# Optimization experiments

Hardware: AMD Instinct MI355X
Metric: run time of the kernel (lower is better)

Reference implementation:

```python
import jax, jax.numpy as jnp
import numpy as np

N, C, E, K = 50000, 128, 640000, 40  # nodes, feat dim, edges, classes
EPS = 1e-5


def setup_inputs() -> dict:
    key = jax.random.key(0)
    ks = jax.random.split(key, 8)
    s = 1.0 / np.sqrt(C)
    return {
        "x": jax.random.normal(ks[0], (N, C), jnp.float32),
        "edge_index": jax.random.randint(ks[1], (2, E), 0, N, dtype=jnp.int32),
        "W_conv": jax.random.normal(ks[2], (C, C), jnp.float32) * s,
        "b_conv": jnp.zeros((C,), jnp.float32),
        "gamma": jnp.ones((C,), jnp.float32),
        "beta": jnp.zeros((C,), jnp.float32),
        "W_fc": jax.random.normal(ks[3], (C, K), jnp.float32) * s,
        "b_fc": jnp.zeros((K,), jnp.float32),
    }


def reference(x, edge_index, W_conv, b_conv, gamma, beta, W_fc, b_fc):
    n = x.shape[0]
    loops = jnp.arange(n, dtype=edge_index.dtype)
    src = jnp.concatenate([edge_index[0], loops])  # add self-loops (PyG default)
    dst = jnp.concatenate([edge_index[1], loops])
    # symmetric normalization: deg^{-1/2}[src] * deg^{-1/2}[dst]
    deg = jax.ops.segment_sum(jnp.ones_like(dst, jnp.float32), dst, num_segments=n)
    dinv = jax.lax.rsqrt(jnp.maximum(deg, 1.0))  # deg >= 1 with self-loops
    norm = dinv[src] * dinv[dst]  # [E+N]
    h = x @ W_conv  # [N, C] transform before propagate (GCNConv)
    agg = jax.ops.segment_sum(h[src] * norm[:, None], dst, num_segments=n) + b_conv
    a = jax.nn.relu(agg) * x  # dropout = identity (eval mode); elementwise mul with residual
    mu = jnp.mean(a, axis=-1, keepdims=True)
    var = jnp.mean((a - mu) ** 2, axis=-1, keepdims=True)
    ln = (a - mu) * jax.lax.rsqrt(var + EPS) * gamma + beta
    return (ln + x) @ W_fc + b_fc
```

## Files before the change

### kernel.cpp

```cpp
#include <hip/hip_runtime.h>

#define C_DIM 128
#define EPS 1e-5f
#define DEG_CAP 64
#define NSCAT 625

typedef __attribute__((ext_vector_type(8))) short short8;
typedef __attribute__((ext_vector_type(4))) float f32x4;

__device__ __forceinline__ unsigned bf16rn(float f) {
    unsigned u = __float_as_uint(f);
    return (u + 0x7fffu + ((u >> 16) & 1u)) >> 16;
}
__device__ __forceinline__ unsigned pack_bf16(float lo, float hi) {
    return bf16rn(lo) | (bf16rn(hi) << 16);
}
__device__ __forceinline__ float blo(unsigned u) { return __uint_as_float(u << 16); }
__device__ __forceinline__ float bhi(unsigned u) { return __uint_as_float(u & 0xffff0000u); }

__global__ __launch_bounds__(256, 4) void fat(const float* __restrict__ x,
                                              const float* __restrict__ W,
                                              unsigned* __restrict__ hb,
                                              const float* __restrict__ Wfc,
                                              unsigned short* __restrict__ WT,
                                              const int* __restrict__ esrc,
                                              const int* __restrict__ edst,
                                              int* __restrict__ cnt,
                                              int* __restrict__ bsrc,
                                              int n, int e, int g1) {
    __shared__ float xT[32][133];
    __shared__ float ws[32][133];
    int b = blockIdx.x;
    int t = threadIdx.x;

    if (b < NSCAT) {
        const int S = NSCAT * 256;
        int i0 = b * 256 + t;
        int i1 = i0 + S, i2 = i1 + S, i3 = i2 + S;
        int d0 = edst[i0], d1 = edst[i1], d2 = edst[i2], d3 = edst[i3];
        int s0 = esrc[i0], s1 = esrc[i1], s2 = esrc[i2], s3 = esrc[i3];
        int p0 = atomicAdd(&cnt[d0], 1);
        int p1 = atomicAdd(&cnt[d1], 1);
        int p2 = atomicAdd(&cnt[d2], 1);
        int p3 = atomicAdd(&cnt[d3], 1);
        if (p0 < DEG_CAP) __builtin_nontemporal_store(s0, &bsrc[(long)d0 * DEG_CAP + p0]);
        if (p1 < DEG_CAP) __builtin_nontemporal_store(s1, &bsrc[(long)d1 * DEG_CAP + p1]);
        if (p2 < DEG_CAP) __builtin_nontemporal_store(s2, &bsrc[(long)d2 * DEG_CAP + p2]);
        if (p3 < DEG_CAP) __builtin_nontemporal_store(s3, &bsrc[(long)d3 * DEG_CAP + p3]);
    } else if (b < NSCAT + g1) {
        int r0 = (b - NSCAT) * 128;
        int w = t >> 6, lane = t & 63;
        int wr = (w >> 1) * 64, wc = (w & 1) * 64;
        int lr = (lane >> 3) * 8, lc = (lane & 7) * 8;
        float acc[8][8] = {};
        for (int kc = 0; kc < 128; kc += 32) {
            __syncthreads();
#pragma unroll
            for (int i = 0; i < 4; i++) {
                int idx = t + i * 256;
                int r = idx >> 3;
                int k4 = (idx & 7) << 2;
                float4 v = make_float4(0.f, 0.f, 0.f, 0.f);
                if (r0 + r < n) v = *(const float4*)&x[(long)(r0 + r) * C_DIM + kc + k4];
                xT[k4 + 0][r] = v.x; xT[k4 + 1][r] = v.y; xT[k4 + 2][r] = v.z; xT[k4 + 3][r] = v.w;
            }
#pragma unroll
            for (int i = 0; i < 4; i++) {
                int idx = t + i * 256;
                int k = idx >> 5;
                int c4 = (idx & 31) << 2;
                *(float4*)&ws[k][c4] = *(const float4*)&W[(long)(kc + k) * C_DIM + c4];
            }
            __syncthreads();
#pragma unroll 4
            for (int k = 0; k < 32; k++) {
                float a[8], bb[8];
                *(float4*)&a[0] = *(float4*)&xT[k][wr + lr];
                *(float4*)&a[4] = *(float4*)&xT[k][wr + lr + 4];
                *(float4*)&bb[0] = *(float4*)&ws[k][wc + lc];
                *(float4*)&bb[4] = *(float4*)&ws[k][wc + lc + 4];
#pragma unroll
                for (int i = 0; i < 8; i++)
#pragma unroll
                    for (int j = 0; j < 8; j++)
                        acc[i][j] += a[i] * bb[j];
            }
        }
#pragma unroll
        for (int i = 0; i < 8; i++) {
            int r = r0 + wr + lr + i;
            if (r < n) {
                uint4 p;
                p.x = pack_bf16(acc[i][0], acc[i][1]);
                p.y = pack_bf16(acc[i][2], acc[i][3]);
                p.z = pack_bf16(acc[i][4], acc[i][5]);
                p.w = pack_bf16(acc[i][6], acc[i][7]);
                *(uint4*)&hb[(long)r * 64 + ((wc + lc) >> 1)] = p;
            }
        }
    } else {
        for (int tid = t; tid < 48 * 128; tid += 256) {
            int nc = tid >> 7;
            int k = tid & 127;
            float v = (nc < 40) ? Wfc[k * 40 + nc] : 0.f;
            WT[nc * 128 + k] = (unsigned short)bf16rn(v);
        }
    }
}

__global__ __launch_bounds__(256) void aggregate(const unsigned* __restrict__ hb,
                                                 const float* __restrict__ x,
                                                 const int* __restrict__ cnt,
                                                 const int* __restrict__ bsrc,
                                                 const float* __restrict__ bconv,
                                                 const float* __restrict__ gamma,
                                                 const float* __restrict__ beta,
                                                 unsigned* __restrict__ zb, int n) {
    int wid = (blockIdx.x * blockDim.x + threadIdx.x) >> 6;
    if (wid >= n) return;
    int lane = threadIdx.x & 63;
    int sub = lane & 15, grp = lane >> 4;
    int i = wid;
    int degt = cnt[i];
    float di = rsqrtf((float)degt + 1.0f);
    int deg = degt > DEG_CAP ? DEG_CAP : degt;
    long base = (long)i * DEG_CAP;

    uint4 us = *(const uint4*)(hb + (long)i * 64 + sub * 4);
    float wself = (grp == 0) ? di * di : 0.f;
    float acc[8];
    acc[0] = wself * blo(us.x); acc[1] = wself * bhi(us.x);
    acc[2] = wself * blo(us.y); acc[3] = wself * bhi(us.y);
    acc[4] = wself * blo(us.z); acc[5] = wself * bhi(us.z);
    acc[6] = wself * blo(us.w); acc[7] = wself * bhi(us.w);

    int k = grp;
    for (; k + 4 < deg; k += 8) {
        int s0 = bsrc[base + k];
        int s1 = bsrc[base + k + 4];
        float w0 = rsqrtf((float)cnt[s0] + 1.0f) * di;
        float w1 = rsqrtf((float)cnt[s1] + 1.0f) * di;
        uint4 u0 = *(const uint4*)(hb + (long)s0 * 64 + sub * 4);
        uint4 u1 = *(const uint4*)(hb + (long)s1 * 64 + sub * 4);
        acc[0] += w0 * blo(u0.x); acc[1] += w0 * bhi(u0.x);
        acc[2] += w0 * blo(u0.y); acc[3] += w0 * bhi(u0.y);
        acc[4] += w0 * blo(u0.z); acc[5] += w0 * bhi(u0.z);
        acc[6] += w0 * blo(u0.w); acc[7] += w0 * bhi(u0.w);
        acc[0] += w1 * blo(u1.x); acc[1] += w1 * bhi(u1.x);
        acc[2] += w1 * blo(u1.y); acc[3] += w1 * bhi(u1.y);
        acc[4] += w1 * blo(u1.z); acc[5] += w1 * bhi(u1.z);
        acc[6] += w1 * blo(u1.w); acc[7] += w1 * bhi(u1.w);
    }
    for (; k < deg; k += 4) {
        int s = bsrc[base + k];
        float w = rsqrtf((float)cnt[s] + 1.0f) * di;
        uint4 u = *(const uint4*)(hb + (long)s * 64 + sub * 4);
        acc[0] += w * blo(u.x); acc[1] += w * bhi(u.x);
        acc[2] += w * blo(u.y); acc[3] += w * bhi(u.y);
        acc[4] += w * blo(u.z); acc[5] += w * bhi(u.z);
        acc[6] += w * blo(u.w); acc[7] += w * bhi(u.w);
    }

#pragma unroll
    for (int j = 0; j < 8; j++) {
        acc[j] += __shfl_xor(acc[j], 16);
        acc[j] += __shfl_xor(acc[j], 32);
    }

    float4 bca = *(const float4*)&bconv[sub * 8];
    float4 bcb = *(const float4*)&bconv[sub * 8 + 4];
    float4 xa  = *(const float4*)&x[(long)i * C_DIM + sub * 8];
    float4 xb  = *(const float4*)&x[(long)i * C_DIM + sub * 8 + 4];
    float a[8], xv[8];
    xv[0] = xa.x; xv[1] = xa.y; xv[2] = xa.z; xv[3] = xa.w;
    xv[4] = xb.x; xv[5] = xb.y; xv[6] = xb.z; xv[7] = xb.w;
    float bc[8] = {bca.x, bca.y, bca.z, bca.w, bcb.x, bcb.y, bcb.z, bcb.w};
#pragma unroll
    for (int j = 0; j < 8; j++) a[j] = fmaxf(acc[j] + bc[j], 0.f) * xv[j];

    float s = a[0] + a[1] + a[2] + a[3] + a[4] + a[5] + a[6] + a[7];
#pragma unroll
    for (int off = 1; off < 16; off <<= 1) s += __shfl_xor(s, off);
    float mu = s * (1.0f / 128.0f);
    float d[8], v = 0.f;
#pragma unroll
    for (int j = 0; j < 8; j++) { d[j] = a[j] - mu; v += d[j] * d[j]; }
#pragma unroll
    for (int off = 1; off < 16; off <<= 1) v += __shfl_xor(v, off);
    float inv = rsqrtf(v * (1.0f / 128.0f) + EPS);

    if (grp == 0) {
        float4 ga = *(const float4*)&gamma[sub * 8];
        float4 gb = *(const float4*)&gamma[sub * 8 + 4];
        float4 ba = *(const float4*)&beta[sub * 8];
        float4 bb = *(const float4*)&beta[sub * 8 + 4];
        float g[8] = {ga.x, ga.y, ga.z, ga.w, gb.x, gb.y, gb.z, gb.w};
        float be[8] = {ba.x, ba.y, ba.z, ba.w, bb.x, bb.y, bb.z, bb.w};
        float o[8];
#pragma unroll
        for (int j = 0; j < 8; j++) o[j] = d[j] * inv * g[j] + be[j] + xv[j];
        uint4 p;
        p.x = pack_bf16(o[0], o[1]);
        p.y = pack_bf16(o[2], o[3]);
        p.z = pack_bf16(o[4], o[5]);
        p.w = pack_bf16(o[6], o[7]);
        *(uint4*)(zb + (long)i * 64 + sub * 4) = p;
    }
}

__global__ __launch_bounds__(256) void gemm2(const unsigned short* __restrict__ zb,
                                             const unsigned short* __restrict__ WT,
                                             const float* __restrict__ bfc,
                                             float* __restrict__ out, int n) {
    int t = threadIdx.x;
    int w = t >> 6, lane = t & 63;
    int r0 = (blockIdx.x * 4 + w) * 64;
    if (r0 >= n) return;
    int mrow = lane & 15;
    int quad = lane >> 4;
    f32x4 acc[4][3];
#pragma unroll
    for (int m = 0; m < 4; m++)
#pragma unroll
        for (int nt = 0; nt < 3; nt++) acc[m][nt] = (f32x4){0.f, 0.f, 0.f, 0.f};
#pragma unroll
    for (int ks = 0; ks < 4; ks++) {
        short8 A[4], B[3];
#pragma unroll
        for (int m = 0; m < 4; m++) {
            int r = r0 + m * 16 + mrow;
            if (r >= n) r = n - 1;
            A[m] = *(const short8*)&zb[(long)r * 128 + ks * 32 + quad * 8];
        }
#pragma unroll
        for (int nt = 0; nt < 3; nt++)
            B[nt] = *(const short8*)&WT[(nt * 16 + mrow) * 128 + ks * 32 + quad * 8];
#pragma unroll
        for (int m = 0; m < 4; m++)
#pragma unroll
            for (int nt = 0; nt < 3; nt++)
                acc[m][nt] = __builtin_amdgcn_mfma_f32_16x16x32_bf16(A[m], B[nt], acc[m][nt], 0, 0, 0);
    }
#pragma unroll
    for (int nt = 0; nt < 3; nt++) {
        int c = nt * 16 + mrow;
        if (c < 40) {
            float bias = bfc[c];
#pragma unroll
            for (int m = 0; m < 4; m++) {
#pragma unroll
                for (int reg = 0; reg < 4; reg++) {
                    int r = r0 + m * 16 + quad * 4 + reg;
                    if (r < n) out[(long)r * 40 + c] = acc[m][nt][reg] + bias;
                }
            }
        }
    }
}

extern "C" void kernel_launch(void* const* d_in, const int* in_sizes, int n_in,
                              void* d_out, int out_size, void* d_ws, size_t ws_size,
                              hipStream_t stream) {
    const float* x     = (const float*)d_in[0];
    const int*   ei    = (const int*)d_in[1];
    const float* Wc    = (const float*)d_in[2];
    const float* bc    = (const float*)d_in[3];
    const float* gamma = (const float*)d_in[4];
    const float* beta  = (const float*)d_in[5];
    const float* Wfc   = (const float*)d_in[6];
    const float* bfc   = (const float*)d_in[7];
    float* out = (float*)d_out;

    int N = in_sizes[0] / C_DIM;
    int E = in_sizes[1] / 2;
    const int* esrc = ei;
    const int* edst = ei + E;

    char* p = (char*)d_ws;
    auto carve = [&](size_t bytes) {
        void* q = (void*)p;
        p += (bytes + 255) & ~(size_t)255;
        return q;
    };
    unsigned* hb       = (unsigned*)carve((size_t)N * 64 * 4);
    unsigned* zb       = (unsigned*)carve((size_t)N * 64 * 4);
    unsigned short* WT = (unsigned short*)carve(48 * 128 * 2);
    int*   cnt         = (int*)carve((size_t)N * 4);
    int*   bsrc        = (int*)carve((size_t)N * DEG_CAP * 4);

    (void)hipMemsetAsync(cnt, 0, (size_t)N * 4, stream);

    int g1 = (N + 127) / 128;
    fat<<<NSCAT + g1 + 1, 256, 0, stream>>>(x, Wc, hb, Wfc, WT, esrc, edst, cnt, bsrc,
                                            N, E, g1);

    aggregate<<<((size_t)N * 64 + 255) / 256, 256, 0, stream>>>(
        hb, x, cnt, bsrc, bc, gamma, beta, zb, N);

    gemm2<<<(N / 64 + 4) / 4, 256, 0, stream>>>((const unsigned short*)zb, WT, bfc, out, N);
}
```

Before: 196.8 us.

## Use bf16 MFMA for feature transform, pad degree counters, precompute dinv

```diff
diff --git a/kernel.cpp b/kernel.cpp
--- a/kernel.cpp
+++ b/kernel.cpp
@@ -18,18 +18,28 @@
 __device__ __forceinline__ float blo(unsigned u) { return __uint_as_float(u << 16); }
 __device__ __forceinline__ float bhi(unsigned u) { return __uint_as_float(u & 0xffff0000u); }
 
-__global__ __launch_bounds__(256, 4) void fat(const float* __restrict__ x,
-                                              const float* __restrict__ W,
-                                              unsigned* __restrict__ hb,
-                                              const float* __restrict__ Wfc,
-                                              unsigned short* __restrict__ WT,
-                                              const int* __restrict__ esrc,
-                                              const int* __restrict__ edst,
-                                              int* __restrict__ cnt,
-                                              int* __restrict__ bsrc,
-                                              int n, int e, int g1) {
-    __shared__ float xT[32][133];
-    __shared__ float ws[32][133];
+__global__ void prep(const float* __restrict__ Wc, const float* __restrict__ Wfc,
+                     unsigned short* __restrict__ WcT, unsigned short* __restrict__ WT) {
+    int tid = blockIdx.x * 256 + threadIdx.x;
+    if (tid < 128 * 128) {
+        int nc = tid >> 7, k = tid & 127;
+        WcT[tid] = (unsigned short)bf16rn(Wc[k * C_DIM + nc]);
+    } else if (tid < 128 * 128 + 48 * 128) {
+        int t2 = tid - 128 * 128;
+        int nc = t2 >> 7, k = t2 & 127;
+        float v = (nc < 40) ? Wfc[k * 40 + nc] : 0.f;
+        WT[t2] = (unsigned short)bf16rn(v);
+    }
+}
+
+__global__ void fat(const float* __restrict__ x,
+                    const unsigned short* __restrict__ WcT,
+                    unsigned* __restrict__ hb,
+                    const int* __restrict__ esrc,
+                    const int* __restrict__ edst,
+                    int* __restrict__ cnt16,
+                    int* __restrict__ bsrc,
+                    int n) {
     int b = blockIdx.x;
     int t = threadIdx.x;
 
@@ -39,79 +49,79 @@
         int i1 = i0 + S, i2 = i1 + S, i3 = i2 + S;
         int d0 = edst[i0], d1 = edst[i1], d2 = edst[i2], d3 = edst[i3];
         int s0 = esrc[i0], s1 = esrc[i1], s2 = esrc[i2], s3 = esrc[i3];
-        int p0 = atomicAdd(&cnt[d0], 1);
-        int p1 = atomicAdd(&cnt[d1], 1);
-        int p2 = atomicAdd(&cnt[d2], 1);
-        int p3 = atomicAdd(&cnt[d3], 1);
+        int p0 = atomicAdd(&cnt16[d0 * 16], 1);
+        int p1 = atomicAdd(&cnt16[d1 * 16], 1);
+        int p2 = atomicAdd(&cnt16[d2 * 16], 1);
+        int p3 = atomicAdd(&cnt16[d3 * 16], 1);
         if (p0 < DEG_CAP) __builtin_nontemporal_store(s0, &bsrc[(long)d0 * DEG_CAP + p0]);
         if (p1 < DEG_CAP) __builtin_nontemporal_store(s1, &bsrc[(long)d1 * DEG_CAP + p1]);
         if (p2 < DEG_CAP) __builtin_nontemporal_store(s2, &bsrc[(long)d2 * DEG_CAP + p2]);
         if (p3 < DEG_CAP) __builtin_nontemporal_store(s3, &bsrc[(long)d3 * DEG_CAP + p3]);
-    } else if (b < NSCAT + g1) {
-        int r0 = (b - NSCAT) * 128;
+    } else {
+        int gb = b - NSCAT;
         int w = t >> 6, lane = t & 63;
-        int wr = (w >> 1) * 64, wc = (w & 1) * 64;
-        int lr = (lane >> 3) * 8, lc = (lane & 7) * 8;
-        float acc[8][8] = {};
-        for (int kc = 0; kc < 128; kc += 32) {
-            __syncthreads();
-#pragma unroll
-            for (int i = 0; i < 4; i++) {
-                int idx = t + i * 256;
-                int r = idx >> 3;
-                int k4 = (idx & 7) << 2;
-                float4 v = make_float4(0.f, 0.f, 0.f, 0.f);
-                if (r0 + r < n) v = *(const float4*)&x[(long)(r0 + r) * C_DIM + kc + k4];
-                xT[k4 + 0][r] = v.x; xT[k4 + 1][r] = v.y; xT[k4 + 2][r] = v.z; xT[k4 + 3][r] = v.w;
+        int rw = gb * 128 + w * 32;
+        if (rw >= n) return;
+        int mrow = lane & 15, quad = lane >> 4;
+        f32x4 acc[2][8];
+#pragma unroll
+        for (int m = 0; m < 2; m++)
+#pragma unroll
+            for (int nt = 0; nt < 8; nt++) acc[m][nt] = (f32x4){0.f, 0.f, 0.f, 0.f};
+        int r0 = rw + mrow;
+        int r1 = rw + 16 + mrow;
+        if (r0 >= n) r0 = n - 1;
+        if (r1 >= n) r1 = n - 1;
+#pragma unroll
+        for (int ks = 0; ks < 4; ks++) {
+            short8 A[2];
+#pragma unroll
+            for (int m = 0; m < 2; m++) {
+                const float* px = &x[(long)(m ? r1 : r0) * C_DIM + ks * 32 + quad * 8];
+                float4 xa = *(const float4*)px;
+                float4 xb = *(const float4*)(px + 4);
+                uint4 au;
+                au.x = pack_bf16(xa.x, xa.y);
+                au.y = pack_bf16(xa.z, xa.w);
+                au.z = pack_bf16(xb.x, xb.y);
+                au.w = pack_bf16(xb.z, xb.w);
+                union { uint4 u; short8 s; } cv;
+                cv.u = au;
+                A[m] = cv.s;
             }
 #pragma unroll
-            for (int i = 0; i < 4; i++) {
-                int idx = t + i * 256;
-                int k = idx >> 5;
-                int c4 = (idx & 31) << 2;
-                *(float4*)&ws[k][c4] = *(const float4*)&W[(long)(kc + k) * C_DIM + c4];
-            }
-            __syncthreads();
-#pragma unroll 4
-            for (int k = 0; k < 32; k++) {
-                float a[8], bb[8];
-                *(float4*)&a[0] = *(float4*)&xT[k][wr + lr];
-                *(float4*)&a[4] = *(float4*)&xT[k][wr + lr + 4];
-                *(float4*)&bb[0] = *(float4*)&ws[k][wc + lc];
-                *(float4*)&bb[4] = *(float4*)&ws[k][wc + lc + 4];
-#pragma unroll
-                for (int i = 0; i < 8; i++)
-#pragma unroll
-                    for (int j = 0; j < 8; j++)
-                        acc[i][j] += a[i] * bb[j];
+            for (int nt = 0; nt < 8; nt++) {
+                short8 B = *(const short8*)&WcT[(nt * 16 + mrow) * 128 + ks * 32 + quad * 8];
+                acc[0][nt] = __builtin_amdgcn_mfma_f32_16x16x32_bf16(A[0], B, acc[0][nt], 0, 0, 0);
+                acc[1][nt] = __builtin_amdgcn_mfma_f32_16x16x32_bf16(A[1], B, acc[1][nt], 0, 0, 0);
             }
         }
-#pragma unroll
-        for (int i = 0; i < 8; i++) {
-            int r = r0 + wr + lr + i;
-            if (r < n) {
-                uint4 p;
-                p.x = pack_bf16(acc[i][0], acc[i][1]);
-                p.y = pack_bf16(acc[i][2], acc[i][3]);
-                p.z = pack_bf16(acc[i][4], acc[i][5]);
-                p.w = pack_bf16(acc[i][6], acc[i][7]);
-                *(uint4*)&hb[(long)r * 64 + ((wc + lc) >> 1)] = p;
-            }
-        }
-    } else {
-        for (int tid = t; tid < 48 * 128; tid += 256) {
-            int nc = tid >> 7;
-            int k = tid & 127;
-            float v = (nc < 40) ? Wfc[k * 40 + nc] : 0.f;
-            WT[nc * 128 + k] = (unsigned short)bf16rn(v);
-        }
-    }
+        bool evenc = (mrow & 1) == 0;
+#pragma unroll
+        for (int m = 0; m < 2; m++)
+#pragma unroll
+            for (int nt = 0; nt < 8; nt++)
+#pragma unroll
+                for (int reg = 0; reg < 4; reg++) {
+                    float v = acc[m][nt][reg];
+                    float pv = __shfl_xor(v, 1);
+                    int rr = rw + m * 16 + quad * 4 + reg;
+                    if (evenc && rr < n)
+                        hb[(long)rr * 64 + ((nt * 16 + mrow) >> 1)] = pack_bf16(v, pv);
+                }
+    }
+}
+
+__global__ void dinv_k(const int* __restrict__ cnt16, float* __restrict__ dinv, int n) {
+    int i = blockIdx.x * blockDim.x + threadIdx.x;
+    if (i < n) dinv[i] = rsqrtf((float)cnt16[i * 16] + 1.0f);
 }
 
 __global__ __launch_bounds__(256) void aggregate(const unsigned* __restrict__ hb,
                                                  const float* __restrict__ x,
-                                                 const int* __restrict__ cnt,
+                                                 const int* __restrict__ cnt16,
                                                  const int* __restrict__ bsrc,
+                                                 const float* __restrict__ dinv,
                                                  const float* __restrict__ bconv,
                                                  const float* __restrict__ gamma,
                                                  const float* __restrict__ beta,
@@ -121,8 +131,8 @@
     int lane = threadIdx.x & 63;
     int sub = lane & 15, grp = lane >> 4;
     int i = wid;
-    int degt = cnt[i];
-    float di = rsqrtf((float)degt + 1.0f);
+    int degt = cnt16[i * 16];
+    float di = dinv[i];
     int deg = degt > DEG_CAP ? DEG_CAP : degt;
     long base = (long)i * DEG_CAP;
 
@@ -138,8 +148,8 @@
     for (; k + 4 < deg; k += 8) {
         int s0 = bsrc[base + k];
         int s1 = bsrc[base + k + 4];
-        float w0 = rsqrtf((float)cnt[s0] + 1.0f) * di;
-        float w1 = rsqrtf((float)cnt[s1] + 1.0f) * di;
+        float w0 = dinv[s0] * di;
+        float w1 = dinv[s1] * di;
         uint4 u0 = *(const uint4*)(hb + (long)s0 * 64 + sub * 4);
         uint4 u1 = *(const uint4*)(hb + (long)s1 * 64 + sub * 4);
         acc[0] += w0 * blo(u0.x); acc[1] += w0 * bhi(u0.x);
@@ -153,7 +163,7 @@
     }
     for (; k < deg; k += 4) {
         int s = bsrc[base + k];
-        float w = rsqrtf((float)cnt[s] + 1.0f) * di;
+        float w = dinv[s] * di;
         uint4 u = *(const uint4*)(hb + (long)s * 64 + sub * 4);
         acc[0] += w * blo(u.x); acc[1] += w * bhi(u.x);
         acc[2] += w * blo(u.y); acc[3] += w * bhi(u.y);
@@ -275,6 +285,7 @@
     int E = in_sizes[1] / 2;
     const int* esrc = ei;
     const int* edst = ei + E;
+    (void)E;
 
     char* p = (char*)d_ws;
     auto carve = [&](size_t bytes) {
@@ -282,20 +293,25 @@
         p += (bytes + 255) & ~(size_t)255;
         return q;
     };
-    unsigned* hb       = (unsigned*)carve((size_t)N * 64 * 4);
-    unsigned* zb       = (unsigned*)carve((size_t)N * 64 * 4);
-    unsigned short* WT = (unsigned short*)carve(48 * 128 * 2);
-    int*   cnt         = (int*)carve((size_t)N * 4);
-    int*   bsrc        = (int*)carve((size_t)N * DEG_CAP * 4);
-
-    (void)hipMemsetAsync(cnt, 0, (size_t)N * 4, stream);
+    unsigned* hb        = (unsigned*)carve((size_t)N * 64 * 4);
+    unsigned* zb        = (unsigned*)carve((size_t)N * 64 * 4);
+    unsigned short* WcT = (unsigned short*)carve(128 * 128 * 2);
+    unsigned short* WT  = (unsigned short*)carve(48 * 128 * 2);
+    float* dinv         = (float*)carve((size_t)N * 4);
+    int*   cnt16        = (int*)carve((size_t)N * 64);
+    int*   bsrc         = (int*)carve((size_t)N * DEG_CAP * 4);
+
+    (void)hipMemsetAsync(cnt16, 0, (size_t)N * 64, stream);
+
+    prep<<<(128 * 128 + 48 * 128 + 255) / 256, 256, 0, stream>>>(Wc, Wfc, WcT, WT);
 
     int g1 = (N + 127) / 128;
-    fat<<<NSCAT + g1 + 1, 256, 0, stream>>>(x, Wc, hb, Wfc, WT, esrc, edst, cnt, bsrc,
-                                            N, E, g1);
+    fat<<<NSCAT + g1, 256, 0, stream>>>(x, WcT, hb, esrc, edst, cnt16, bsrc, N);
+
+    dinv_k<<<(N + 255) / 256, 256, 0, stream>>>(cnt16, dinv, N);
 
     aggregate<<<((size_t)N * 64 + 255) / 256, 256, 0, stream>>>(
-        hb, x, cnt, bsrc, bc, gamma, beta, zb, N);
+        hb, x, cnt16, bsrc, dinv, bc, gamma, beta, zb, N);
 
     gemm2<<<(N / 64 + 4) / 4, 256, 0, stream>>>((const unsigned short*)zb, WT, bfc, out, N);
 }
```

Measured after the change: 185.6 us. 5.7% less time.
